# Kernel optimization log

Hardware: AMD Instinct MI355X
Metric: run time of the kernel (lower is better)

## Reference

```python
import jax, jax.numpy as jnp
import numpy as np

B, T, D, H, V = 16, 256, 256, 512, 32000  # batch, seq_len, input_dim, hidden, vocab


def setup_inputs() -> dict:
    key = jax.random.key(0)
    ks = jax.random.split(key, 9)
    g = lambda k, shape, scale: (jax.random.normal(k, shape, jnp.float32) * scale)
    return {
        "images": g(ks[0], (B, D), 1.0),
        "labels": jax.random.randint(ks[1], (T, B), 0, V, dtype=jnp.int64),
        "embed_table": g(ks[2], (V, D), 0.02),
        "W_ih": g(ks[3], (4 * H, D), 1.0 / np.sqrt(H)),
        "W_hh": g(ks[4], (4 * H, H), 1.0 / np.sqrt(H)),
        "b_ih": g(ks[5], (4 * H,), 0.01),
        "b_hh": g(ks[6], (4 * H,), 0.01),
        "W_fc": g(ks[7], (V, H), 1.0 / np.sqrt(H)),
        "b_fc": g(ks[8], (V,), 0.01),
    }


def reference(images, labels, embed_table, W_ih, W_hh, b_ih, b_hh, W_fc, b_fc):
    # labels: (T, B) -> embedded (T, B, D); t=0 consumes images instead
    lab_emb = embed_table[labels]                               # (T, B, D)
    x_seq = jnp.concatenate([images[None], lab_emb[1:]], 0)     # (T, B, D)
    # precompute input-side gate contributions for all timesteps (one big GEMM)
    x_gates = jnp.einsum("tbd,gd->tbg", x_seq, W_ih) + b_ih + b_hh  # (T, B, 4H)

    hidden = W_hh.shape[1]
    bsz = images.shape[0]

    def step(carry, xg):
        h, c = carry
        gates = xg + h @ W_hh.T                                 # (B, 4H)
        i, f, g_, o = jnp.split(gates, 4, axis=-1)
        c = jax.nn.sigmoid(f) * c + jax.nn.sigmoid(i) * jnp.tanh(g_)
        h = jax.nn.sigmoid(o) * jnp.tanh(c)
        return (h, c), h

    init = (jnp.zeros((bsz, hidden), x_gates.dtype),
            jnp.zeros((bsz, hidden), x_gates.dtype))
    _, hs = jax.lax.scan(step, init, x_gates)                   # hs: (T, B, H)
    # fc_out applied to every timestep's hidden state
    return jnp.einsum("tbh,vh->tbv", hs, W_fc) + b_fc           # (T, B, V)
```

## Files before the change

kernel.cpp:

```cpp
#include <hip/hip_runtime.h>

typedef __attribute__((ext_vector_type(8))) short short8;
typedef __attribute__((ext_vector_type(4))) float f32x4;
typedef unsigned int uint;
typedef unsigned short ushort;

#define T_ 256
#define B_ 16
#define D_ 256
#define H_ 512
#define V_ 32000
#define GH 2048
#define SENT 0xFFFFFFFFu

__device__ __forceinline__ ushort f2bf(float f) {
    uint u = __float_as_uint(f);
    u += 0x7FFFu + ((u >> 16) & 1u);
    return (ushort)(u >> 16);
}

__device__ __forceinline__ float fsig(float x) {
    return 1.0f / (1.0f + __expf(-x));
}

__device__ __forceinline__ float ftanh(float x) {
    float a = __expf(-2.0f * fabsf(x));
    float t = (1.0f - a) / (1.0f + a);
    return x >= 0.0f ? t : -t;
}

__device__ __forceinline__ void cvt4(const float* s, ushort* d) {
    float4 v = *(const float4*)s;
    ushort4 o;
    o.x = f2bf(v.x); o.y = f2bf(v.y); o.z = f2bf(v.z); o.w = f2bf(v.w);
    *(ushort4*)d = o;
}

__global__ void prep_convert(const float* __restrict__ Wih, const float* __restrict__ Whh,
                             const float* __restrict__ Wfc, const float* __restrict__ bih,
                             const float* __restrict__ bhh,
                             ushort* __restrict__ dWih, ushort* __restrict__ dWhh,
                             ushort* __restrict__ dWfc, float* __restrict__ bsum) {
    const long nA = (long)GH * D_ / 4;
    const long nB = (long)GH * H_ / 4;
    const long nC = (long)V_ * H_ / 4;
    const long nS = GH / 4;
    long i = (long)blockIdx.x * blockDim.x + threadIdx.x;
    if (i >= nA + nB + nC + nS) return;
    if (i < nA) {
        cvt4(Wih + i * 4, dWih + i * 4);
    } else if (i < nA + nB) {
        long j = i - nA;
        cvt4(Whh + j * 4, dWhh + j * 4);
    } else if (i < nA + nB + nC) {
        long j = i - nA - nB;
        cvt4(Wfc + j * 4, dWfc + j * 4);
    } else {
        long j = (i - nA - nB - nC) * 4;
        float4 a = *(const float4*)(bih + j);
        float4 b = *(const float4*)(bhh + j);
        float4 o;
        o.x = a.x + b.x; o.y = a.y + b.y; o.z = a.z + b.z; o.w = a.w + b.w;
        *(float4*)(bsum + j) = o;
    }
}

__global__ void prep_xseq(const float* __restrict__ images, const int* __restrict__ labels,
                          const float* __restrict__ embed, ushort* __restrict__ xseq) {
    int m = blockIdx.x;
    int l = threadIdx.x;
    int t = m >> 4, b = m & 15;
    const float* src = (t == 0) ? (images + b * D_) : (embed + (long)labels[m] * D_);
    cvt4(src + l * 4, xseq + (long)m * D_ + l * 4);
}

template <int K>
__global__ __launch_bounds__(256) void gemm_bt(const ushort* __restrict__ A,
                                               const ushort* __restrict__ Bw,
                                               float* __restrict__ C,
                                               const float* __restrict__ bias,
                                               int ldc) {
    __shared__ ushort As[128 * 64];
    __shared__ ushort Bs[128 * 64];
    const int tid = threadIdx.x;
    const int lane = tid & 63;
    const int w = tid >> 6;
    const int wr = w >> 1, wc = w & 1;
    const long mBase = (long)blockIdx.x * 128;
    const long nBase = (long)blockIdx.y * 128;

    f32x4 acc[4][4];
#pragma unroll
    for (int i = 0; i < 4; ++i)
#pragma unroll
        for (int j = 0; j < 4; ++j) acc[i][j] = (f32x4){0.f, 0.f, 0.f, 0.f};

    const char* Ab = (const char*)A;
    const char* Bb = (const char*)Bw;

    for (int kk = 0; kk < K / 64; ++kk) {
#pragma unroll
        for (int it = 0; it < 4; ++it) {
            int c = w * 4 + it;
            int r = c * 8 + (lane >> 3);
            int sg = (lane & 7) ^ (r & 7);
            long aoff = (mBase + r) * (long)(K * 2) + kk * 128 + sg * 16;
            long boff = (nBase + r) * (long)(K * 2) + kk * 128 + sg * 16;
            __builtin_amdgcn_global_load_lds(
                (const __attribute__((address_space(1))) void*)(Ab + aoff),
                (__attribute__((address_space(3))) void*)((char*)As + c * 1024), 16, 0, 0);
            __builtin_amdgcn_global_load_lds(
                (const __attribute__((address_space(1))) void*)(Bb + boff),
                (__attribute__((address_space(3))) void*)((char*)Bs + c * 1024), 16, 0, 0);
        }
        __syncthreads();
#pragma unroll
        for (int k2 = 0; k2 < 2; ++k2) {
            short8 af[4], bfr[4];
#pragma unroll
            for (int mi = 0; mi < 4; ++mi) {
                int mrow = wr * 64 + mi * 16 + (lane & 15);
                int g = (k2 * 4 + (lane >> 4)) ^ (mrow & 7);
                af[mi] = *(const short8*)((const char*)As + mrow * 128 + g * 16);
            }
#pragma unroll
            for (int ni = 0; ni < 4; ++ni) {
                int nrow = wc * 64 + ni * 16 + (lane & 15);
                int g = (k2 * 4 + (lane >> 4)) ^ (nrow & 7);
                bfr[ni] = *(const short8*)((const char*)Bs + nrow * 128 + g * 16);
            }
#pragma unroll
            for (int mi = 0; mi < 4; ++mi)
#pragma unroll
                for (int ni = 0; ni < 4; ++ni)
                    acc[mi][ni] = __builtin_amdgcn_mfma_f32_16x16x32_bf16(
                        af[mi], bfr[ni], acc[mi][ni], 0, 0, 0);
        }
        __syncthreads();
    }
#pragma unroll
    for (int ni = 0; ni < 4; ++ni) {
        long col = nBase + wc * 64 + ni * 16 + (lane & 15);
        float bv = bias[col];
#pragma unroll
        for (int mi = 0; mi < 4; ++mi) {
            long row0 = mBase + wr * 64 + mi * 16 + ((lane >> 4) << 2);
#pragma unroll
            for (int rr = 0; rr < 4; ++rr)
                C[(row0 + rr) * (long)ldc + col] = acc[mi][ni][rr] + bv;
        }
    }
}

__global__ __launch_bounds__(256) void lstm_scan(const ushort* __restrict__ Whh,
                                                 const float* __restrict__ xg,
                                                 ushort* __restrict__ hs) {
    __shared__ ushort Ws[64 * 512];
    __shared__ ushort hb[16 * 512];
    __shared__ float gb[4][16][16];
    __shared__ ushort hloc[16][16];

    const int tid = threadIdx.x;
    const int lane = tid & 63;
    const int w = tid >> 6;
    const int g = blockIdx.x;

#pragma unroll
    for (int j = 0; j < 16; ++j) {
        int gid = j * 256 + tid;
        int row = gid >> 6;
        int gcol = gid & 63;
        int srow = (row >> 4) * H_ + g * 16 + (row & 15);
        uint4 v = *(const uint4*)(Whh + (long)srow * H_ + gcol * 8);
        int dg = gcol ^ (row & 7);
        *(uint4*)((char*)Ws + row * 1024 + dg * 16) = v;
    }
    __syncthreads();

    const int b = tid >> 4;
    const int jj = tid & 15;
    const int row = tid >> 4;
    const int c0 = tid & 15;
    float cst = 0.0f;

    for (int t = 0; t < T_; ++t) {
        long xb = ((long)t * B_ + b) * GH + g * 16 + jj;
        float gi = xg[xb];
        float gf = xg[xb + 512];
        float gg = xg[xb + 1024];
        float go = xg[xb + 1536];

        if (t > 0) {
            uint vals[16];
#pragma unroll
            for (int j = 0; j < 16; ++j) {
                int u = c0 + j * 16;
                if ((u >> 3) == g)
                    vals[j] = (uint)hloc[row][(u & 7) * 2] |
                              ((uint)hloc[row][(u & 7) * 2 + 1] << 16);
                else
                    vals[j] = SENT;
            }
            uint* hsrcU = (uint*)hs + ((long)(t - 1) * (B_ * H_)) / 2 + row * 256;
            int guard = 0;
            for (;;) {
                int pend = 0;
#pragma unroll
                for (int j = 0; j < 16; ++j) {
                    if (vals[j] == SENT)
                        vals[j] = __hip_atomic_load(hsrcU + c0 + j * 16,
                                                    __ATOMIC_RELAXED, __HIP_MEMORY_SCOPE_AGENT);
                }
#pragma unroll
                for (int j = 0; j < 16; ++j) pend += (vals[j] == SENT) ? 1 : 0;
                if (pend == 0 || ++guard > (1 << 20)) break;
            }
#pragma unroll
            for (int j = 0; j < 16; ++j) {
                int u = c0 + j * 16;
                int gcol = u >> 2, sub = u & 3;
                int dg = gcol ^ (row & 7);
                *(uint*)((char*)hb + row * 1024 + dg * 16 + sub * 4) = vals[j];
            }
            __syncthreads();
            f32x4 acc0 = (f32x4){0.f, 0.f, 0.f, 0.f};
            f32x4 acc1 = (f32x4){0.f, 0.f, 0.f, 0.f};
            const int arow = lane & 15;
            const int brow = w * 16 + (lane & 15);
#pragma unroll
            for (int k0 = 0; k0 < 16; k0 += 2) {
                int ga0 = (k0 * 4 + (lane >> 4)) ^ (arow & 7);
                int gB0 = (k0 * 4 + (lane >> 4)) ^ (brow & 7);
                int ga1 = ((k0 + 1) * 4 + (lane >> 4)) ^ (arow & 7);
                int gB1 = ((k0 + 1) * 4 + (lane >> 4)) ^ (brow & 7);
                short8 a0 = *(const short8*)((const char*)hb + arow * 1024 + ga0 * 16);
                short8 b0 = *(const short8*)((const char*)Ws + brow * 1024 + gB0 * 16);
                short8 a1 = *(const short8*)((const char*)hb + arow * 1024 + ga1 * 16);
                short8 b1 = *(const short8*)((const char*)Ws + brow * 1024 + gB1 * 16);
                acc0 = __builtin_amdgcn_mfma_f32_16x16x32_bf16(a0, b0, acc0, 0, 0, 0);
                acc1 = __builtin_amdgcn_mfma_f32_16x16x32_bf16(a1, b1, acc1, 0, 0, 0);
            }
#pragma unroll
            for (int r = 0; r < 4; ++r)
                gb[w][((lane >> 4) << 2) + r][lane & 15] = acc0[r] + acc1[r];
            __syncthreads();
            gi += gb[0][b][jj];
            gf += gb[1][b][jj];
            gg += gb[2][b][jj];
            go += gb[3][b][jj];
        }
        float ii = fsig(gi), ff = fsig(gf), oo = fsig(go), tg = ftanh(gg);
        cst = ff * cst + ii * tg;
        float hv = oo * ftanh(cst);
        ushort hb16 = f2bf(hv);
        hloc[b][jj] = hb16;
        uint mybits = (uint)hb16;
        uint partner = (uint)__shfl_xor((int)mybits, 1);
        if ((jj & 1) == 0) {
            uint val = mybits | (partner << 16);
            uint* dst = (uint*)hs + ((long)t * B_ + b) * (H_ / 2) + (g * 16 + jj) / 2;
            __hip_atomic_store(dst, val, __ATOMIC_RELAXED, __HIP_MEMORY_SCOPE_AGENT);
        }
        __syncthreads();
    }
}

extern "C" void kernel_launch(void* const* d_in, const int* in_sizes, int n_in,
                              void* d_out, int out_size, void* d_ws, size_t ws_size,
                              hipStream_t stream) {
    const float* images = (const float*)d_in[0];
    const int* labels   = (const int*)d_in[1];
    const float* embed  = (const float*)d_in[2];
    const float* Wih    = (const float*)d_in[3];
    const float* Whh    = (const float*)d_in[4];
    const float* bih    = (const float*)d_in[5];
    const float* bhh    = (const float*)d_in[6];
    const float* Wfc    = (const float*)d_in[7];
    const float* bfc    = (const float*)d_in[8];
    float* out = (float*)d_out;

    char* p = (char*)d_ws;
    ushort* dWfc = (ushort*)p; p += (long)V_ * H_ * 2;
    ushort* dWih = (ushort*)p; p += (long)GH * D_ * 2;
    ushort* dWhh = (ushort*)p; p += (long)GH * H_ * 2;
    ushort* xseq = (ushort*)p; p += (long)T_ * B_ * D_ * 2;
    float* xg    = (float*)p;  p += (long)T_ * B_ * GH * 4;
    ushort* hs   = (ushort*)p; p += (long)T_ * B_ * H_ * 2;
    float* bsum  = (float*)p;  p += GH * 4;

    hipMemsetAsync(hs, 0xFF, (size_t)T_ * B_ * H_ * 2, stream);

    {
        long total = (long)GH * D_ / 4 + (long)GH * H_ / 4 + (long)V_ * H_ / 4 + GH / 4;
        int blocks = (int)((total + 255) / 256);
        prep_convert<<<blocks, 256, 0, stream>>>(Wih, Whh, Wfc, bih, bhh, dWih, dWhh, dWfc, bsum);
    }
    prep_xseq<<<T_ * B_, 64, 0, stream>>>(images, labels, embed, xseq);

    gemm_bt<D_><<<dim3(32, 16), 256, 0, stream>>>(xseq, dWih, xg, bsum, GH);

    lstm_scan<<<32, 256, 0, stream>>>(dWhh, xg, hs);

    gemm_bt<H_><<<dim3(32, 250), 256, 0, stream>>>(hs, dWfc, out, bfc, V_);
}
```

Measured before the change: 897.4 us.

## Interleave gate rows in LSTM scan to keep gate combine in-register via shuffles

Reorders the W_hh rows staged in shared memory so each wave's MFMA output tile holds all four gates (i,f,g,o) for its own hidden units. Gate values are then combined with cross-lane shuffles instead of a shared-memory gate buffer and an extra __syncthreads, and the trailing per-step barrier is removed. Local hidden values are no longer reused from shared memory; every block polls all of h(t-1) from global memory. This shortens the serial per-timestep critical path, but it adds shuffle and select work and more global polling traffic, and dropping the barrier could cause a hazard when hb is rewritten at the next step.

```diff
diff --git a/kernel.cpp b/kernel.cpp
--- a/kernel.cpp
+++ b/kernel.cpp
@@ -157,8 +157,6 @@
                                                  ushort* __restrict__ hs) {
     __shared__ ushort Ws[64 * 512];
     __shared__ ushort hb[16 * 512];
-    __shared__ float gb[4][16][16];
-    __shared__ ushort hloc[16][16];
 
     const int tid = threadIdx.x;
     const int lane = tid & 63;
@@ -170,57 +168,55 @@
         int gid = j * 256 + tid;
         int row = gid >> 6;
         int gcol = gid & 63;
-        int srow = (row >> 4) * H_ + g * 16 + (row & 15);
+        int srow = (row & 3) * H_ + g * 16 + (row >> 2);
         uint4 v = *(const uint4*)(Whh + (long)srow * H_ + gcol * 8);
         int dg = gcol ^ (row & 7);
         *(uint4*)((char*)Ws + row * 1024 + dg * 16) = v;
     }
     __syncthreads();
 
-    const int b = tid >> 4;
-    const int jj = tid & 15;
-    const int row = tid >> 4;
-    const int c0 = tid & 15;
+    const int gl  = lane & 3;
+    const int jlp = (lane >> 2) & 3;
+    const int rg  = lane >> 4;
+    const int b   = rg * 4 + gl;
+    const int colg = g * 16 + w * 4 + jlp;
+    const int prow = tid >> 4;
+    const int c0   = tid & 15;
+
     float cst = 0.0f;
 
     for (int t = 0; t < T_; ++t) {
-        long xb = ((long)t * B_ + b) * GH + g * 16 + jj;
+        long xb = ((long)t * B_ + b) * GH + colg;
         float gi = xg[xb];
         float gf = xg[xb + 512];
         float gg = xg[xb + 1024];
         float go = xg[xb + 1536];
 
         if (t > 0) {
+            uint* hsrcU = (uint*)hs + ((long)(t - 1) * (B_ * H_)) / 2 + prow * 256;
             uint vals[16];
 #pragma unroll
-            for (int j = 0; j < 16; ++j) {
-                int u = c0 + j * 16;
-                if ((u >> 3) == g)
-                    vals[j] = (uint)hloc[row][(u & 7) * 2] |
-                              ((uint)hloc[row][(u & 7) * 2 + 1] << 16);
-                else
-                    vals[j] = SENT;
-            }
-            uint* hsrcU = (uint*)hs + ((long)(t - 1) * (B_ * H_)) / 2 + row * 256;
+            for (int j = 0; j < 16; ++j)
+                vals[j] = __hip_atomic_load(hsrcU + c0 + j * 16,
+                                            __ATOMIC_RELAXED, __HIP_MEMORY_SCOPE_AGENT);
             int guard = 0;
             for (;;) {
                 int pend = 0;
 #pragma unroll
-                for (int j = 0; j < 16; ++j) {
+                for (int j = 0; j < 16; ++j) pend += (vals[j] == SENT) ? 1 : 0;
+                if (pend == 0 || ++guard > (1 << 20)) break;
+#pragma unroll
+                for (int j = 0; j < 16; ++j)
                     if (vals[j] == SENT)
                         vals[j] = __hip_atomic_load(hsrcU + c0 + j * 16,
                                                     __ATOMIC_RELAXED, __HIP_MEMORY_SCOPE_AGENT);
-                }
-#pragma unroll
-                for (int j = 0; j < 16; ++j) pend += (vals[j] == SENT) ? 1 : 0;
-                if (pend == 0 || ++guard > (1 << 20)) break;
             }
 #pragma unroll
             for (int j = 0; j < 16; ++j) {
                 int u = c0 + j * 16;
                 int gcol = u >> 2, sub = u & 3;
-                int dg = gcol ^ (row & 7);
-                *(uint*)((char*)hb + row * 1024 + dg * 16 + sub * 4) = vals[j];
+                int dg = gcol ^ (prow & 7);
+                *(uint*)((char*)hb + prow * 1024 + dg * 16 + sub * 4) = vals[j];
             }
             __syncthreads();
             f32x4 acc0 = (f32x4){0.f, 0.f, 0.f, 0.f};
@@ -240,28 +236,40 @@
                 acc0 = __builtin_amdgcn_mfma_f32_16x16x32_bf16(a0, b0, acc0, 0, 0, 0);
                 acc1 = __builtin_amdgcn_mfma_f32_16x16x32_bf16(a1, b1, acc1, 0, 0, 0);
             }
-#pragma unroll
-            for (int r = 0; r < 4; ++r)
-                gb[w][((lane >> 4) << 2) + r][lane & 15] = acc0[r] + acc1[r];
-            __syncthreads();
-            gi += gb[0][b][jj];
-            gf += gb[1][b][jj];
-            gg += gb[2][b][jj];
-            go += gb[3][b][jj];
+            f32x4 acc;
+#pragma unroll
+            for (int r = 0; r < 4; ++r) acc[r] = acc0[r] + acc1[r];
+            f32x4 x1;
+#pragma unroll
+            for (int r = 0; r < 4; ++r) x1[r] = __shfl_xor(acc[r], 1);
+            f32x4 lo = (gl & 1) ? x1 : acc;
+            f32x4 hi = (gl & 1) ? acc : x1;
+            f32x4 lo2, hi2;
+#pragma unroll
+            for (int r = 0; r < 4; ++r) {
+                lo2[r] = __shfl_xor(lo[r], 2);
+                hi2[r] = __shfl_xor(hi[r], 2);
+            }
+            f32x4 G0 = (gl & 2) ? lo2 : lo;
+            f32x4 G1 = (gl & 2) ? hi2 : hi;
+            f32x4 G2 = (gl & 2) ? lo : lo2;
+            f32x4 G3 = (gl & 2) ? hi : hi2;
+            float s0 = (gl & 2) ? ((gl & 1) ? G0[3] : G0[2]) : ((gl & 1) ? G0[1] : G0[0]);
+            float s1 = (gl & 2) ? ((gl & 1) ? G1[3] : G1[2]) : ((gl & 1) ? G1[1] : G1[0]);
+            float s2 = (gl & 2) ? ((gl & 1) ? G2[3] : G2[2]) : ((gl & 1) ? G2[1] : G2[0]);
+            float s3 = (gl & 2) ? ((gl & 1) ? G3[3] : G3[2]) : ((gl & 1) ? G3[1] : G3[0]);
+            gi += s0; gf += s1; gg += s2; go += s3;
         }
         float ii = fsig(gi), ff = fsig(gf), oo = fsig(go), tg = ftanh(gg);
         cst = ff * cst + ii * tg;
         float hv = oo * ftanh(cst);
-        ushort hb16 = f2bf(hv);
-        hloc[b][jj] = hb16;
-        uint mybits = (uint)hb16;
-        uint partner = (uint)__shfl_xor((int)mybits, 1);
-        if ((jj & 1) == 0) {
-            uint val = mybits | (partner << 16);
-            uint* dst = (uint*)hs + ((long)t * B_ + b) * (H_ / 2) + (g * 16 + jj) / 2;
+        uint hbits = (uint)f2bf(hv);
+        uint pbits = (uint)__shfl_xor((int)hbits, 4);
+        if ((lane & 4) == 0) {
+            uint val = hbits | (pbits << 16);
+            uint* dst = (uint*)hs + ((long)t * B_ + b) * (H_ / 2) + (colg >> 1);
             __hip_atomic_store(dst, val, __ATOMIC_RELAXED, __HIP_MEMORY_SCOPE_AGENT);
         }
-        __syncthreads();
     }
 }
 
```

Result: slower. 1.087 ms (+21.1%).

## Fuse LSTM scan with output projection GEMM using a dynamic tile queue

Applied to the files above, without the earlier changes.

Merges the recurrent scan and the vocabulary projection GEMM into one persistent kernel. The first 32 blocks run the scan while the other 224 blocks pull output tiles from an atomic counter. Each worker spins until the hidden states for its 8-timestep row block are published, so the FC GEMM overlaps the serial recurrence instead of waiting for it to finish. The scan also keeps its own hidden slice in LDS instead of re-reading it through hloc. The cost is atomic per-element loads for the A tile instead of async loads, plus spin-waiting workers that compete with the scan blocks for bandwidth.

```diff
diff --git a/kernel.cpp b/kernel.cpp
--- a/kernel.cpp
+++ b/kernel.cpp
@@ -12,6 +12,7 @@
 #define V_ 32000
 #define GH 2048
 #define SENT 0xFFFFFFFFu
+#define NTILE (32u * 250u)
 
 __device__ __forceinline__ ushort f2bf(float f) {
     uint u = __float_as_uint(f);
@@ -34,6 +35,10 @@
     ushort4 o;
     o.x = f2bf(v.x); o.y = f2bf(v.y); o.z = f2bf(v.z); o.w = f2bf(v.w);
     *(ushort4*)d = o;
+}
+
+__device__ __forceinline__ uint aload(const uint* p) {
+    return __hip_atomic_load(p, __ATOMIC_RELAXED, __HIP_MEMORY_SCOPE_AGENT);
 }
 
 __global__ void prep_convert(const float* __restrict__ Wih, const float* __restrict__ Whh,
@@ -152,116 +157,227 @@
     }
 }
 
-__global__ __launch_bounds__(256) void lstm_scan(const ushort* __restrict__ Whh,
-                                                 const float* __restrict__ xg,
-                                                 ushort* __restrict__ hs) {
-    __shared__ ushort Ws[64 * 512];
-    __shared__ ushort hb[16 * 512];
-    __shared__ float gb[4][16][16];
-    __shared__ ushort hloc[16][16];
+__global__ __launch_bounds__(256) void fused_scan_fc(const ushort* __restrict__ Whh,
+                                                     const float* __restrict__ xg,
+                                                     ushort* __restrict__ hs,
+                                                     const ushort* __restrict__ Wfc,
+                                                     const float* __restrict__ bfc,
+                                                     float* __restrict__ out,
+                                                     uint* __restrict__ counter) {
+    __shared__ union {
+        struct { ushort Ws[64 * 512]; ushort hb[16 * 512]; float gb[4][16][16]; } s;
+        struct { ushort As[128 * 64]; ushort Bs[128 * 64]; uint tileShare; } f;
+    } u;
 
     const int tid = threadIdx.x;
     const int lane = tid & 63;
     const int w = tid >> 6;
-    const int g = blockIdx.x;
-
-#pragma unroll
-    for (int j = 0; j < 16; ++j) {
-        int gid = j * 256 + tid;
-        int row = gid >> 6;
-        int gcol = gid & 63;
-        int srow = (row >> 4) * H_ + g * 16 + (row & 15);
-        uint4 v = *(const uint4*)(Whh + (long)srow * H_ + gcol * 8);
-        int dg = gcol ^ (row & 7);
-        *(uint4*)((char*)Ws + row * 1024 + dg * 16) = v;
-    }
-    __syncthreads();
-
-    const int b = tid >> 4;
-    const int jj = tid & 15;
-    const int row = tid >> 4;
-    const int c0 = tid & 15;
-    float cst = 0.0f;
-
-    for (int t = 0; t < T_; ++t) {
-        long xb = ((long)t * B_ + b) * GH + g * 16 + jj;
-        float gi = xg[xb];
-        float gf = xg[xb + 512];
-        float gg = xg[xb + 1024];
-        float go = xg[xb + 1536];
-
-        if (t > 0) {
-            uint vals[16];
-#pragma unroll
-            for (int j = 0; j < 16; ++j) {
-                int u = c0 + j * 16;
-                if ((u >> 3) == g)
-                    vals[j] = (uint)hloc[row][(u & 7) * 2] |
-                              ((uint)hloc[row][(u & 7) * 2 + 1] << 16);
-                else
-                    vals[j] = SENT;
-            }
-            uint* hsrcU = (uint*)hs + ((long)(t - 1) * (B_ * H_)) / 2 + row * 256;
-            int guard = 0;
-            for (;;) {
-                int pend = 0;
+
+    if (blockIdx.x < 32) {
+        const int g = blockIdx.x;
+#pragma unroll
+        for (int j = 0; j < 16; ++j) {
+            int gid = j * 256 + tid;
+            int row = gid >> 6;
+            int gcol = gid & 63;
+            int srow = (row >> 4) * H_ + g * 16 + (row & 15);
+            uint4 v = *(const uint4*)(Whh + (long)srow * H_ + gcol * 8);
+            int dg = gcol ^ (row & 7);
+            *(uint4*)((char*)u.s.Ws + row * 1024 + dg * 16) = v;
+        }
+        __syncthreads();
+
+        const int b = tid >> 4;
+        const int jj = tid & 15;
+        float cst = 0.0f;
+
+        for (int t = 0; t < T_; ++t) {
+            long xb = ((long)t * B_ + b) * GH + g * 16 + jj;
+            float gi = xg[xb];
+            float gf = xg[xb + 512];
+            float gg = xg[xb + 1024];
+            float go = xg[xb + 1536];
+
+            if (t > 0) {
+                uint* hsrcU = (uint*)hs + ((long)(t - 1) * (B_ * H_)) / 2 + b * 256;
+                uint vals[16];
 #pragma unroll
                 for (int j = 0; j < 16; ++j) {
-                    if (vals[j] == SENT)
-                        vals[j] = __hip_atomic_load(hsrcU + c0 + j * 16,
-                                                    __ATOMIC_RELAXED, __HIP_MEMORY_SCOPE_AGENT);
-                }
-#pragma unroll
-                for (int j = 0; j < 16; ++j) pend += (vals[j] == SENT) ? 1 : 0;
-                if (pend == 0 || ++guard > (1 << 20)) break;
-            }
-#pragma unroll
-            for (int j = 0; j < 16; ++j) {
-                int u = c0 + j * 16;
-                int gcol = u >> 2, sub = u & 3;
-                int dg = gcol ^ (row & 7);
-                *(uint*)((char*)hb + row * 1024 + dg * 16 + sub * 4) = vals[j];
-            }
+                    int u2 = jj + j * 16;
+                    vals[j] = ((u2 >> 3) == g) ? 0u : aload(hsrcU + u2);
+                }
+                int guard = 0;
+                for (;;) {
+                    int pend = 0;
+#pragma unroll
+                    for (int j = 0; j < 16; ++j) pend += (vals[j] == SENT) ? 1 : 0;
+                    if (pend == 0 || ++guard > (1 << 20)) break;
+#pragma unroll
+                    for (int j = 0; j < 16; ++j)
+                        if (vals[j] == SENT)
+                            vals[j] = aload(hsrcU + jj + j * 16);
+                }
+#pragma unroll
+                for (int j = 0; j < 16; ++j) {
+                    int u2 = jj + j * 16;
+                    if ((u2 >> 3) != g) {
+                        int gcol = u2 >> 2, sub = u2 & 3;
+                        int dg = gcol ^ (b & 7);
+                        *(uint*)((char*)u.s.hb + b * 1024 + dg * 16 + sub * 4) = vals[j];
+                    }
+                }
+                __syncthreads();
+                f32x4 acc0 = (f32x4){0.f, 0.f, 0.f, 0.f};
+                f32x4 acc1 = (f32x4){0.f, 0.f, 0.f, 0.f};
+                const int arow = lane & 15;
+                const int brow = w * 16 + (lane & 15);
+#pragma unroll
+                for (int k0 = 0; k0 < 16; k0 += 2) {
+                    int ga0 = (k0 * 4 + (lane >> 4)) ^ (arow & 7);
+                    int gB0 = (k0 * 4 + (lane >> 4)) ^ (brow & 7);
+                    int ga1 = ((k0 + 1) * 4 + (lane >> 4)) ^ (arow & 7);
+                    int gB1 = ((k0 + 1) * 4 + (lane >> 4)) ^ (brow & 7);
+                    short8 a0 = *(const short8*)((const char*)u.s.hb + arow * 1024 + ga0 * 16);
+                    short8 b0 = *(const short8*)((const char*)u.s.Ws + brow * 1024 + gB0 * 16);
+                    short8 a1 = *(const short8*)((const char*)u.s.hb + arow * 1024 + ga1 * 16);
+                    short8 b1 = *(const short8*)((const char*)u.s.Ws + brow * 1024 + gB1 * 16);
+                    acc0 = __builtin_amdgcn_mfma_f32_16x16x32_bf16(a0, b0, acc0, 0, 0, 0);
+                    acc1 = __builtin_amdgcn_mfma_f32_16x16x32_bf16(a1, b1, acc1, 0, 0, 0);
+                }
+#pragma unroll
+                for (int r = 0; r < 4; ++r)
+                    u.s.gb[w][((lane >> 4) << 2) + r][lane & 15] = acc0[r] + acc1[r];
+                __syncthreads();
+                gi += u.s.gb[0][b][jj];
+                gf += u.s.gb[1][b][jj];
+                gg += u.s.gb[2][b][jj];
+                go += u.s.gb[3][b][jj];
+            }
+            float ii = fsig(gi), ff = fsig(gf), oo = fsig(go), tg = ftanh(gg);
+            cst = ff * cst + ii * tg;
+            float hv = oo * ftanh(cst);
+            ushort hbv = f2bf(hv);
+            {
+                int colb = (g * 16 + jj) * 2;
+                int gcol = colb >> 4;
+                int dg = gcol ^ (b & 7);
+                *(ushort*)((char*)u.s.hb + b * 1024 + dg * 16 + (colb & 15)) = hbv;
+            }
+            uint hbits = (uint)hbv;
+            uint pbits = (uint)__shfl_xor((int)hbits, 1);
+            if ((jj & 1) == 0) {
+                uint val = hbits | (pbits << 16);
+                uint* dst = (uint*)hs + ((long)t * B_ + b) * (H_ / 2) + (g * 16 + jj) / 2;
+                __hip_atomic_store(dst, val, __ATOMIC_RELAXED, __HIP_MEMORY_SCOPE_AGENT);
+            }
+        }
+    } else {
+        const int wr = w >> 1, wc = w & 1;
+        const char* Bb = (const char*)Wfc;
+        const uint* hsU = (const uint*)hs;
+        int last_valid = -1;
+
+        for (;;) {
             __syncthreads();
-            f32x4 acc0 = (f32x4){0.f, 0.f, 0.f, 0.f};
-            f32x4 acc1 = (f32x4){0.f, 0.f, 0.f, 0.f};
-            const int arow = lane & 15;
-            const int brow = w * 16 + (lane & 15);
-#pragma unroll
-            for (int k0 = 0; k0 < 16; k0 += 2) {
-                int ga0 = (k0 * 4 + (lane >> 4)) ^ (arow & 7);
-                int gB0 = (k0 * 4 + (lane >> 4)) ^ (brow & 7);
-                int ga1 = ((k0 + 1) * 4 + (lane >> 4)) ^ (arow & 7);
-                int gB1 = ((k0 + 1) * 4 + (lane >> 4)) ^ (brow & 7);
-                short8 a0 = *(const short8*)((const char*)hb + arow * 1024 + ga0 * 16);
-                short8 b0 = *(const short8*)((const char*)Ws + brow * 1024 + gB0 * 16);
-                short8 a1 = *(const short8*)((const char*)hb + arow * 1024 + ga1 * 16);
-                short8 b1 = *(const short8*)((const char*)Ws + brow * 1024 + gB1 * 16);
-                acc0 = __builtin_amdgcn_mfma_f32_16x16x32_bf16(a0, b0, acc0, 0, 0, 0);
-                acc1 = __builtin_amdgcn_mfma_f32_16x16x32_bf16(a1, b1, acc1, 0, 0, 0);
-            }
-#pragma unroll
-            for (int r = 0; r < 4; ++r)
-                gb[w][((lane >> 4) << 2) + r][lane & 15] = acc0[r] + acc1[r];
+            if (tid == 0) u.f.tileShare = atomicAdd(counter, 1u);
             __syncthreads();
-            gi += gb[0][b][jj];
-            gf += gb[1][b][jj];
-            gg += gb[2][b][jj];
-            go += gb[3][b][jj];
-        }
-        float ii = fsig(gi), ff = fsig(gf), oo = fsig(go), tg = ftanh(gg);
-        cst = ff * cst + ii * tg;
-        float hv = oo * ftanh(cst);
-        ushort hb16 = f2bf(hv);
-        hloc[b][jj] = hb16;
-        uint mybits = (uint)hb16;
-        uint partner = (uint)__shfl_xor((int)mybits, 1);
-        if ((jj & 1) == 0) {
-            uint val = mybits | (partner << 16);
-            uint* dst = (uint*)hs + ((long)t * B_ + b) * (H_ / 2) + (g * 16 + jj) / 2;
-            __hip_atomic_store(dst, val, __ATOMIC_RELAXED, __HIP_MEMORY_SCOPE_AGENT);
-        }
-        __syncthreads();
+            uint tile = u.f.tileShare;
+            if (tile >= NTILE) break;
+            int m = (int)(tile / 250u);
+            int n = (int)(tile % 250u);
+
+            if (m > last_valid) {
+                uint* base = (uint*)hs + ((long)(m * 8 + 7) * (B_ * H_)) / 2 + (tid >> 4) * 256;
+                const int c0 = tid & 15;
+                uint vals[16];
+#pragma unroll
+                for (int j = 0; j < 16; ++j) vals[j] = aload(base + c0 + j * 16);
+                int guard = 0;
+                for (;;) {
+                    int pend = 0;
+#pragma unroll
+                    for (int j = 0; j < 16; ++j) pend += (vals[j] == SENT) ? 1 : 0;
+                    if (pend == 0 || ++guard > (1 << 17)) break;
+                    __builtin_amdgcn_s_sleep(127);
+                    __builtin_amdgcn_s_sleep(127);
+#pragma unroll
+                    for (int j = 0; j < 16; ++j)
+                        if (vals[j] == SENT) vals[j] = aload(base + c0 + j * 16);
+                }
+                last_valid = m;
+                __syncthreads();
+            }
+
+            const long mBase = (long)m * 128;
+            const long nBase = (long)n * 128;
+            f32x4 acc[4][4];
+#pragma unroll
+            for (int i = 0; i < 4; ++i)
+#pragma unroll
+                for (int j = 0; j < 4; ++j) acc[i][j] = (f32x4){0.f, 0.f, 0.f, 0.f};
+
+            for (int kk = 0; kk < 8; ++kk) {
+#pragma unroll
+                for (int q = 0; q < 4; ++q) {
+                    int gi2 = q * 256 + tid;
+                    int r = gi2 >> 3, lgr = gi2 & 7;
+                    int sgr = lgr ^ (r & 7);
+                    long src = (mBase + r) * (long)(H_ / 2) + kk * 32 + sgr * 4;
+                    uint4 vv;
+                    vv.x = aload(hsU + src + 0);
+                    vv.y = aload(hsU + src + 1);
+                    vv.z = aload(hsU + src + 2);
+                    vv.w = aload(hsU + src + 3);
+                    *(uint4*)((char*)u.f.As + gi2 * 16) = vv;
+                }
+#pragma unroll
+                for (int it = 0; it < 4; ++it) {
+                    int c = w * 4 + it;
+                    int r = c * 8 + (lane >> 3);
+                    int sg = (lane & 7) ^ (r & 7);
+                    long boff = (nBase + r) * (long)(H_ * 2) + kk * 128 + sg * 16;
+                    __builtin_amdgcn_global_load_lds(
+                        (const __attribute__((address_space(1))) void*)(Bb + boff),
+                        (__attribute__((address_space(3))) void*)((char*)u.f.Bs + c * 1024), 16, 0, 0);
+                }
+                __syncthreads();
+#pragma unroll
+                for (int k2 = 0; k2 < 2; ++k2) {
+                    short8 af[4], bfr[4];
+#pragma unroll
+                    for (int mi = 0; mi < 4; ++mi) {
+                        int mrow = wr * 64 + mi * 16 + (lane & 15);
+                        int gg2 = (k2 * 4 + (lane >> 4)) ^ (mrow & 7);
+                        af[mi] = *(const short8*)((const char*)u.f.As + mrow * 128 + gg2 * 16);
+                    }
+#pragma unroll
+                    for (int ni = 0; ni < 4; ++ni) {
+                        int nrow = wc * 64 + ni * 16 + (lane & 15);
+                        int gg2 = (k2 * 4 + (lane >> 4)) ^ (nrow & 7);
+                        bfr[ni] = *(const short8*)((const char*)u.f.Bs + nrow * 128 + gg2 * 16);
+                    }
+#pragma unroll
+                    for (int mi = 0; mi < 4; ++mi)
+#pragma unroll
+                        for (int ni = 0; ni < 4; ++ni)
+                            acc[mi][ni] = __builtin_amdgcn_mfma_f32_16x16x32_bf16(
+                                af[mi], bfr[ni], acc[mi][ni], 0, 0, 0);
+                }
+                __syncthreads();
+            }
+#pragma unroll
+            for (int ni = 0; ni < 4; ++ni) {
+                long col = nBase + wc * 64 + ni * 16 + (lane & 15);
+                float bv = bfc[col];
+#pragma unroll
+                for (int mi = 0; mi < 4; ++mi) {
+                    long row0 = mBase + wr * 64 + mi * 16 + ((lane >> 4) << 2);
+#pragma unroll
+                    for (int rr = 0; rr < 4; ++rr)
+                        out[(row0 + rr) * (long)V_ + col] = acc[mi][ni][rr] + bv;
+                }
+            }
+        }
     }
 }
 
@@ -287,8 +403,10 @@
     float* xg    = (float*)p;  p += (long)T_ * B_ * GH * 4;
     ushort* hs   = (ushort*)p; p += (long)T_ * B_ * H_ * 2;
     float* bsum  = (float*)p;  p += GH * 4;
+    uint* counter = (uint*)p;  p += 256;
 
     hipMemsetAsync(hs, 0xFF, (size_t)T_ * B_ * H_ * 2, stream);
+    hipMemsetAsync(counter, 0, sizeof(uint), stream);
 
     {
         long total = (long)GH * D_ / 4 + (long)GH * H_ / 4 + (long)V_ * H_ / 4 + GH / 4;
@@ -299,7 +417,5 @@
 
     gemm_bt<D_><<<dim3(32, 16), 256, 0, stream>>>(xseq, dWih, xg, bsum, GH);
 
-    lstm_scan<<<32, 256, 0, stream>>>(dWhh, xg, hs);
-
-    gemm_bt<H_><<<dim3(32, 250), 256, 0, stream>>>(hs, dWfc, out, bfc, V_);
-}
+    fused_scan_fc<<<256, 256, 0, stream>>>(dWhh, xg, hs, dWfc, bfc, out, counter);
+}
```

Result: slower. 1.155 ms (+28.7%).

## Load h directly into MFMA registers and drop LDS staging and barriers

Applied to the files above, without the earlier changes.

Each wave now loads the previous timestep's hidden-state fragments from global memory straight into the MFMA A-operand registers and polls each fragment for the sentinel separately. This removes the LDS staging buffer for h, the local hloc copy, and two __syncthreads per timestep, so MFMAs can start as soon as their own fragments arrive. The cost is that every wave loads all of h redundantly, four waves instead of one cooperative load. Dropping the end-of-step barrier also relies on the gb barrier alone to protect reuse of the shared gate buffer.

```diff
diff --git a/kernel.cpp b/kernel.cpp
--- a/kernel.cpp
+++ b/kernel.cpp
@@ -34,6 +34,10 @@
     ushort4 o;
     o.x = f2bf(v.x); o.y = f2bf(v.y); o.z = f2bf(v.z); o.w = f2bf(v.w);
     *(ushort4*)d = o;
+}
+
+__device__ __forceinline__ uint aload(const uint* p) {
+    return __hip_atomic_load(p, __ATOMIC_RELAXED, __HIP_MEMORY_SCOPE_AGENT);
 }
 
 __global__ void prep_convert(const float* __restrict__ Wih, const float* __restrict__ Whh,
@@ -156,9 +160,7 @@
                                                  const float* __restrict__ xg,
                                                  ushort* __restrict__ hs) {
     __shared__ ushort Ws[64 * 512];
-    __shared__ ushort hb[16 * 512];
     __shared__ float gb[4][16][16];
-    __shared__ ushort hloc[16][16];
 
     const int tid = threadIdx.x;
     const int lane = tid & 63;
@@ -179,8 +181,9 @@
 
     const int b = tid >> 4;
     const int jj = tid & 15;
-    const int row = tid >> 4;
-    const int c0 = tid & 15;
+    const int arow = lane & 15;
+    const int q = lane >> 4;
+    const int brow = w * 16 + (lane & 15);
     float cst = 0.0f;
 
     for (int t = 0; t < T_; ++t) {
@@ -191,58 +194,45 @@
         float go = xg[xb + 1536];
 
         if (t > 0) {
-            uint vals[16];
+            const uint* hsrc = (const uint*)hs + (long)(t - 1) * (B_ * H_ / 2)
+                               + arow * (H_ / 2) + q * 4;
+            uint a[16][4];
 #pragma unroll
             for (int j = 0; j < 16; ++j) {
-                int u = c0 + j * 16;
-                if ((u >> 3) == g)
-                    vals[j] = (uint)hloc[row][(u & 7) * 2] |
-                              ((uint)hloc[row][(u & 7) * 2 + 1] << 16);
-                else
-                    vals[j] = SENT;
-            }
-            uint* hsrcU = (uint*)hs + ((long)(t - 1) * (B_ * H_)) / 2 + row * 256;
-            int guard = 0;
-            for (;;) {
-                int pend = 0;
-#pragma unroll
-                for (int j = 0; j < 16; ++j) {
-                    if (vals[j] == SENT)
-                        vals[j] = __hip_atomic_load(hsrcU + c0 + j * 16,
-                                                    __ATOMIC_RELAXED, __HIP_MEMORY_SCOPE_AGENT);
-                }
-#pragma unroll
-                for (int j = 0; j < 16; ++j) pend += (vals[j] == SENT) ? 1 : 0;
-                if (pend == 0 || ++guard > (1 << 20)) break;
-            }
-#pragma unroll
-            for (int j = 0; j < 16; ++j) {
-                int u = c0 + j * 16;
-                int gcol = u >> 2, sub = u & 3;
-                int dg = gcol ^ (row & 7);
-                *(uint*)((char*)hb + row * 1024 + dg * 16 + sub * 4) = vals[j];
-            }
-            __syncthreads();
+#pragma unroll
+                for (int d = 0; d < 4; ++d)
+                    a[j][d] = aload(hsrc + j * 16 + d);
+            }
             f32x4 acc0 = (f32x4){0.f, 0.f, 0.f, 0.f};
             f32x4 acc1 = (f32x4){0.f, 0.f, 0.f, 0.f};
-            const int arow = lane & 15;
-            const int brow = w * 16 + (lane & 15);
-#pragma unroll
-            for (int k0 = 0; k0 < 16; k0 += 2) {
-                int ga0 = (k0 * 4 + (lane >> 4)) ^ (arow & 7);
-                int gB0 = (k0 * 4 + (lane >> 4)) ^ (brow & 7);
-                int ga1 = ((k0 + 1) * 4 + (lane >> 4)) ^ (arow & 7);
-                int gB1 = ((k0 + 1) * 4 + (lane >> 4)) ^ (brow & 7);
-                short8 a0 = *(const short8*)((const char*)hb + arow * 1024 + ga0 * 16);
-                short8 b0 = *(const short8*)((const char*)Ws + brow * 1024 + gB0 * 16);
-                short8 a1 = *(const short8*)((const char*)hb + arow * 1024 + ga1 * 16);
-                short8 b1 = *(const short8*)((const char*)Ws + brow * 1024 + gB1 * 16);
-                acc0 = __builtin_amdgcn_mfma_f32_16x16x32_bf16(a0, b0, acc0, 0, 0, 0);
-                acc1 = __builtin_amdgcn_mfma_f32_16x16x32_bf16(a1, b1, acc1, 0, 0, 0);
+#pragma unroll
+            for (int j = 0; j < 16; ++j) {
+                int miss = (a[j][0] == SENT) | (a[j][1] == SENT) |
+                           (a[j][2] == SENT) | (a[j][3] == SENT);
+                int guard = 0;
+                while (__any(miss)) {
+                    if (miss) {
+#pragma unroll
+                        for (int d = 0; d < 4; ++d)
+                            a[j][d] = aload(hsrc + j * 16 + d);
+                    }
+                    miss = (a[j][0] == SENT) | (a[j][1] == SENT) |
+                           (a[j][2] == SENT) | (a[j][3] == SENT);
+                    if (++guard > (1 << 20)) break;
+                }
+                union { uint u[4]; short8 s; } cv;
+                cv.u[0] = a[j][0]; cv.u[1] = a[j][1];
+                cv.u[2] = a[j][2]; cv.u[3] = a[j][3];
+                int gB = (j * 4 + q) ^ (brow & 7);
+                short8 bf = *(const short8*)((const char*)Ws + brow * 1024 + gB * 16);
+                if ((j & 1) == 0)
+                    acc0 = __builtin_amdgcn_mfma_f32_16x16x32_bf16(cv.s, bf, acc0, 0, 0, 0);
+                else
+                    acc1 = __builtin_amdgcn_mfma_f32_16x16x32_bf16(cv.s, bf, acc1, 0, 0, 0);
             }
 #pragma unroll
             for (int r = 0; r < 4; ++r)
-                gb[w][((lane >> 4) << 2) + r][lane & 15] = acc0[r] + acc1[r];
+                gb[w][(q << 2) + r][arow] = acc0[r] + acc1[r];
             __syncthreads();
             gi += gb[0][b][jj];
             gf += gb[1][b][jj];
@@ -252,16 +242,13 @@
         float ii = fsig(gi), ff = fsig(gf), oo = fsig(go), tg = ftanh(gg);
         cst = ff * cst + ii * tg;
         float hv = oo * ftanh(cst);
-        ushort hb16 = f2bf(hv);
-        hloc[b][jj] = hb16;
-        uint mybits = (uint)hb16;
-        uint partner = (uint)__shfl_xor((int)mybits, 1);
+        uint hbits = (uint)f2bf(hv);
+        uint p1 = (uint)__shfl_xor((int)hbits, 1);
         if ((jj & 1) == 0) {
-            uint val = mybits | (partner << 16);
+            uint val = hbits | (p1 << 16);
             uint* dst = (uint*)hs + ((long)t * B_ + b) * (H_ / 2) + (g * 16 + jj) / 2;
             __hip_atomic_store(dst, val, __ATOMIC_RELAXED, __HIP_MEMORY_SCOPE_AGENT);
         }
-        __syncthreads();
     }
 }
 
```

Result: slower. 2.765 ms (+208.1%).
